# Kernel tuning notes

Measured on AMD Instinct MI355X. Metric: run time of the kernel, lower is better.

The kernel has to match this reference:

```python
import jax, jax.numpy as jnp
import numpy as np

MIN_TAU = 0.1
MAX_TAU = 10.0
DT = 0.1
HID = 64
IND = 3
B, N = 4, 262144


def _xavier(key, shape):
    fan_in, fan_out = shape[1], shape[0]
    limit = float(np.sqrt(6.0 / (fan_in + fan_out)))
    return jax.random.uniform(key, shape, jnp.float32, -limit, limit)


def setup_inputs() -> dict:
    key = jax.random.key(0)
    ks = jax.random.split(key, 7)
    h = jax.random.normal(ks[0], (B, N, HID), jnp.float32)
    u = jax.random.normal(ks[1], (B, N, IND), jnp.float32)
    return {
        "h": h,
        "u": u,
        "W_h": _xavier(ks[2], (HID, HID)),
        "U_h": _xavier(ks[3], (HID, IND)),
        "b_h": jnp.zeros((HID,), jnp.float32),
        "W_tau": _xavier(ks[4], (HID, HID)),
        "U_tau": _xavier(ks[5], (HID, IND)),
        "b_tau": jnp.zeros((HID,), jnp.float32),
        "W_out": _xavier(ks[6], (3, HID)),
        "b_out": jnp.zeros((3,), jnp.float32),
    }


def reference(h, u, W_h, U_h, b_h, W_tau, U_tau, b_tau, W_out, b_out):
    # tau: state-dependent time constant (B,N,HID)
    tau_raw = jnp.einsum('bnh,kh->bnk', h, W_tau) + jnp.einsum('bni,ki->bnk', u, U_tau) + b_tau
    tau = MIN_TAU + jax.nn.softplus(tau_raw) * (MAX_TAU - MIN_TAU)
    pre = jnp.einsum('bnh,kh->bnk', h, W_h) + jnp.einsum('bni,ki->bnk', u, U_h) + b_h
    f_h = jax.nn.sigmoid(pre)
    h_new = h + DT * (-h / tau + f_h)
    v = jnp.tanh(jnp.einsum('bnh,oh->bno', h_new, W_out) + b_out)
    return (h_new, v)
```

## Files before the change

### kernel.cpp

```cpp
#include <hip/hip_runtime.h>
#include <hip/hip_bf16.h>
#include <math.h>

#define HID 64
#define DT 0.1f
#define MIN_TAU 0.1f
#define TAU_SCALE 9.9f

#define WSTRIDE 104
#define WROWS   192
#define WELEMS  (WROWS * WSTRIDE)

typedef __attribute__((ext_vector_type(8))) short bf16x8;
typedef __attribute__((ext_vector_type(4))) float f32x4;

__device__ __forceinline__ short f2bf(float f) {
    union { __hip_bfloat16 b; short s; } c;
    c.b = __float2bfloat16(f);
    return c.s;
}
__device__ __forceinline__ float fast_rcp(float x) { return __builtin_amdgcn_rcpf(x); }
__device__ __forceinline__ float fast_tanh(float x) {
    float e = __expf(2.f * x);
    return fmaf(-2.f, fast_rcp(e + 1.f), 1.f);
}

__global__ __launch_bounds__(256) void prep_weights(
    const float* __restrict__ W_tau, const float* __restrict__ U_tau,
    const float* __restrict__ b_tau,
    const float* __restrict__ W_h, const float* __restrict__ U_h,
    const float* __restrict__ b_h,
    short* __restrict__ wbf)
{
    const int idx = blockIdx.x * 256 + threadIdx.x;
    if (idx >= WELEMS) return;
    const int row = idx / WSTRIDE;
    const int c = idx - row * WSTRIDE;
    float val = 0.f;
    if (row < 64) {
        const int r = row;
        if (c < 64)       val = W_tau[r * 64 + c];
        else if (c < 67)  val = U_tau[r * 3 + (c - 64)];
        else if (c == 67) val = b_tau[r];
    } else if (row < 128) {
        const int r = row - 64;
        if (c < 64)       val = W_h[r * 64 + c];
        else if (c < 67)  val = U_h[r * 3 + (c - 64)];
        else if (c == 67) val = b_h[r];
    } else {
        val = (c == row - 128) ? 1.0f : 0.f;
    }
    wbf[idx] = f2bf(val);
}

__global__ __launch_bounds__(256, 2) void liquid_mfma_kernel(
    const float* __restrict__ h, const float* __restrict__ u,
    const short* __restrict__ wbf,
    const float* __restrict__ W_out, const float* __restrict__ b_out,
    float* __restrict__ h_out, float* __restrict__ v_out, int ntiles)
{
    __shared__ short wlds[WELEMS];

    const int tid = threadIdx.x;
    {
        const uint4* s = (const uint4*)wbf;
        uint4* d = (uint4*)wlds;
        for (int i = tid; i < WELEMS / 8; i += 256) d[i] = s[i];
    }

    const int lane = tid & 63;
    const int col  = lane & 15;
    const int quad = lane >> 4;
    const int wid  = tid >> 6;

    float wo[3][4];
#pragma unroll
    for (int o = 0; o < 3; ++o)
#pragma unroll
        for (int nt = 0; nt < 4; ++nt)
            wo[o][nt] = W_out[o * 64 + nt * 16 + col];
    const float bo_sel = (col == 0) ? b_out[0] : ((col == 1) ? b_out[1] : b_out[2]);

    __syncthreads();

    const int tstep = gridDim.x;
    int t = blockIdx.x;

    float4 pf0, pf1, pf2, pf3;
    float pu0 = 0.f, pu1 = 0.f, pu2 = 0.f;

#define LOADA(TT)                                                              \
    do {                                                                       \
        const unsigned q_ = (unsigned)(TT) * 64u + (unsigned)(wid * 16 + col); \
        const float* hp_ = h + q_ * 64u + (unsigned)(quad * 8);                \
        pf0 = *(const float4*)hp_;                                             \
        pf1 = *(const float4*)(hp_ + 4);                                       \
        pf2 = *(const float4*)(hp_ + 32);                                      \
        pf3 = *(const float4*)(hp_ + 36);                                      \
        if (quad == 0) {                                                       \
            const float* up_ = u + q_ * 3u;                                    \
            pu0 = up_[0]; pu1 = up_[1]; pu2 = up_[2];                          \
        }                                                                      \
    } while (0)

    if (t < ntiles) LOADA(t);

    for (; t < ntiles; t += tstep) {
        const unsigned q0 = (unsigned)t * 64u + (unsigned)(wid * 16);

        bf16x8 af0, af1;
        af0[0] = f2bf(pf0.x); af0[1] = f2bf(pf0.y); af0[2] = f2bf(pf0.z); af0[3] = f2bf(pf0.w);
        af0[4] = f2bf(pf1.x); af0[5] = f2bf(pf1.y); af0[6] = f2bf(pf1.z); af0[7] = f2bf(pf1.w);
        af1[0] = f2bf(pf2.x); af1[1] = f2bf(pf2.y); af1[2] = f2bf(pf2.z); af1[3] = f2bf(pf2.w);
        af1[4] = f2bf(pf3.x); af1[5] = f2bf(pf3.y); af1[6] = f2bf(pf3.z); af1[7] = f2bf(pf3.w);

        bf16x8 af2 = (bf16x8)(short)0;
        if (quad == 0) {
            af2[0] = f2bf(pu0); af2[1] = f2bf(pu1); af2[2] = f2bf(pu2);
            af2[3] = f2bf(1.0f);
        }

        const int tn = t + tstep;
        if (tn < ntiles) LOADA(tn);

        f32x4 acc[12];
#pragma unroll
        for (int nt = 0; nt < 12; ++nt) acc[nt] = (f32x4){0.f, 0.f, 0.f, 0.f};

#pragma unroll
        for (int nt = 0; nt < 8; ++nt) {
            const short* wb = &wlds[(nt * 16 + col) * WSTRIDE + quad * 8];
            acc[nt] = __builtin_amdgcn_mfma_f32_16x16x32_bf16(
                af0, *(const bf16x8*)wb, acc[nt], 0, 0, 0);
            acc[nt] = __builtin_amdgcn_mfma_f32_16x16x32_bf16(
                af1, *(const bf16x8*)(wb + 32), acc[nt], 0, 0, 0);
            acc[nt] = __builtin_amdgcn_mfma_f32_16x16x32_bf16(
                af2, *(const bf16x8*)(wb + 64), acc[nt], 0, 0, 0);
        }
#pragma unroll
        for (int nt = 8; nt < 12; ++nt) {
            const short* wb = &wlds[(nt * 16 + col) * WSTRIDE + quad * 8];
            acc[nt] = __builtin_amdgcn_mfma_f32_16x16x32_bf16(
                af0, *(const bf16x8*)wb, acc[nt], 0, 0, 0);
            acc[nt] = __builtin_amdgcn_mfma_f32_16x16x32_bf16(
                af1, *(const bf16x8*)(wb + 32), acc[nt], 0, 0, 0);
        }

#pragma unroll
        for (int r = 0; r < 4; ++r) {
            const unsigned p = q0 + (unsigned)(quad * 4 + r);
            float pv0 = 0.f, pv1 = 0.f, pv2 = 0.f;
#pragma unroll
            for (int ntk = 0; ntk < 4; ++ntk) {
                const float at = acc[ntk][r];
                const float ap = acc[ntk + 4][r];
                const float hk = acc[ntk + 8][r];
                const float sp = fmaxf(at, 0.f) + __logf(1.f + __expf(-fabsf(at)));
                const float tau = fmaf(sp, TAU_SCALE, MIN_TAU);
                const float f = fast_rcp(1.f + __expf(-ap));
                const float hnew = fmaf(DT, f - hk * fast_rcp(tau), hk);
                h_out[p * 64u + (unsigned)(ntk * 16 + col)] = hnew;
                pv0 = fmaf(hnew, wo[0][ntk], pv0);
                pv1 = fmaf(hnew, wo[1][ntk], pv1);
                pv2 = fmaf(hnew, wo[2][ntk], pv2);
            }
#pragma unroll
            for (int s = 1; s < 16; s <<= 1) {
                pv0 += __shfl_xor(pv0, s, 64);
                pv1 += __shfl_xor(pv1, s, 64);
                pv2 += __shfl_xor(pv2, s, 64);
            }
            const float pv = (col == 0) ? pv0 : ((col == 1) ? pv1 : pv2);
            if (col < 3)
                v_out[p * 3u + (unsigned)col] = fast_tanh(pv + bo_sel);
        }
    }
#undef LOADA
}

extern "C" void kernel_launch(void* const* d_in, const int* in_sizes, int n_in,
                              void* d_out, int out_size, void* d_ws, size_t ws_size,
                              hipStream_t stream) {
    const float* h     = (const float*)d_in[0];
    const float* u     = (const float*)d_in[1];
    const float* W_h   = (const float*)d_in[2];
    const float* U_h   = (const float*)d_in[3];
    const float* b_h   = (const float*)d_in[4];
    const float* W_tau = (const float*)d_in[5];
    const float* U_tau = (const float*)d_in[6];
    const float* b_tau = (const float*)d_in[7];
    const float* W_out = (const float*)d_in[8];
    const float* b_out = (const float*)d_in[9];

    const int total = in_sizes[0] / HID;
    float* h_out = (float*)d_out;
    float* v_out = h_out + (size_t)total * HID;

    short* wbf = (short*)d_ws;

    prep_weights<<<(WELEMS + 255) / 256, 256, 0, stream>>>(
        W_tau, U_tau, b_tau, W_h, U_h, b_h, wbf);

    const int ntiles = total / 64;
    const int grid = 1024;
    liquid_mfma_kernel<<<grid, 256, 0, stream>>>(
        h, u, wbf, W_out, b_out, h_out, v_out, ntiles);
}
```

Measured before the change: 147.6 us.

## Hold weight fragments in registers and build identity transpose operands in-register

Weight B-fragments move out of LDS and are loaded once per thread into registers (24 bf16x8 vectors), which removes the LDS staging, the block barrier and the per-tile LDS reads. The identity-matrix MFMAs that transpose h into the accumulator layout now use operands generated in registers, and the wasted k-steps over zero identity columns are dropped (4 MFMAs instead of 8). The cost is a large increase in VGPR use (about 96 extra registers), which could reduce occupancy under launch_bounds(256,2) or cause spills.

```diff
diff --git a/kernel.cpp b/kernel.cpp
--- a/kernel.cpp
+++ b/kernel.cpp
@@ -8,7 +8,7 @@
 #define TAU_SCALE 9.9f
 
 #define WSTRIDE 104
-#define WROWS   192
+#define WROWS   128
 #define WELEMS  (WROWS * WSTRIDE)
 
 typedef __attribute__((ext_vector_type(8))) short bf16x8;
@@ -42,13 +42,11 @@
         if (c < 64)       val = W_tau[r * 64 + c];
         else if (c < 67)  val = U_tau[r * 3 + (c - 64)];
         else if (c == 67) val = b_tau[r];
-    } else if (row < 128) {
+    } else {
         const int r = row - 64;
         if (c < 64)       val = W_h[r * 64 + c];
         else if (c < 67)  val = U_h[r * 3 + (c - 64)];
         else if (c == 67) val = b_h[r];
-    } else {
-        val = (c == row - 128) ? 1.0f : 0.f;
     }
     wbf[idx] = f2bf(val);
 }
@@ -59,20 +57,26 @@
     const float* __restrict__ W_out, const float* __restrict__ b_out,
     float* __restrict__ h_out, float* __restrict__ v_out, int ntiles)
 {
-    __shared__ short wlds[WELEMS];
-
-    const int tid = threadIdx.x;
-    {
-        const uint4* s = (const uint4*)wbf;
-        uint4* d = (uint4*)wlds;
-        for (int i = tid; i < WELEMS / 8; i += 256) d[i] = s[i];
-    }
-
+    const int tid  = threadIdx.x;
     const int lane = tid & 63;
     const int col  = lane & 15;
     const int quad = lane >> 4;
     const int wid  = tid >> 6;
 
+    bf16x8 bw[8][3];
+#pragma unroll
+    for (int nt = 0; nt < 8; ++nt)
+#pragma unroll
+        for (int ks = 0; ks < 3; ++ks)
+            bw[nt][ks] = *(const bf16x8*)&wbf[(nt * 16 + col) * WSTRIDE + ks * 32 + quad * 8];
+
+    bf16x8 idA, idB;
+#pragma unroll
+    for (int e = 0; e < 8; ++e) {
+        idA[e] = (quad * 8 + e == col)      ? (short)0x3F80 : (short)0;
+        idB[e] = (quad * 8 + e == col + 16) ? (short)0x3F80 : (short)0;
+    }
+
     float wo[3][4];
 #pragma unroll
     for (int o = 0; o < 3; ++o)
@@ -80,8 +84,6 @@
         for (int nt = 0; nt < 4; ++nt)
             wo[o][nt] = W_out[o * 64 + nt * 16 + col];
     const float bo_sel = (col == 0) ? b_out[0] : ((col == 1) ? b_out[1] : b_out[2]);
-
-    __syncthreads();
 
     const int tstep = gridDim.x;
     int t = blockIdx.x;
@@ -129,22 +131,14 @@
 
 #pragma unroll
         for (int nt = 0; nt < 8; ++nt) {
-            const short* wb = &wlds[(nt * 16 + col) * WSTRIDE + quad * 8];
-            acc[nt] = __builtin_amdgcn_mfma_f32_16x16x32_bf16(
-                af0, *(const bf16x8*)wb, acc[nt], 0, 0, 0);
-            acc[nt] = __builtin_amdgcn_mfma_f32_16x16x32_bf16(
-                af1, *(const bf16x8*)(wb + 32), acc[nt], 0, 0, 0);
-            acc[nt] = __builtin_amdgcn_mfma_f32_16x16x32_bf16(
-                af2, *(const bf16x8*)(wb + 64), acc[nt], 0, 0, 0);
+            acc[nt] = __builtin_amdgcn_mfma_f32_16x16x32_bf16(af0, bw[nt][0], acc[nt], 0, 0, 0);
+            acc[nt] = __builtin_amdgcn_mfma_f32_16x16x32_bf16(af1, bw[nt][1], acc[nt], 0, 0, 0);
+            acc[nt] = __builtin_amdgcn_mfma_f32_16x16x32_bf16(af2, bw[nt][2], acc[nt], 0, 0, 0);
         }
-#pragma unroll
-        for (int nt = 8; nt < 12; ++nt) {
-            const short* wb = &wlds[(nt * 16 + col) * WSTRIDE + quad * 8];
-            acc[nt] = __builtin_amdgcn_mfma_f32_16x16x32_bf16(
-                af0, *(const bf16x8*)wb, acc[nt], 0, 0, 0);
-            acc[nt] = __builtin_amdgcn_mfma_f32_16x16x32_bf16(
-                af1, *(const bf16x8*)(wb + 32), acc[nt], 0, 0, 0);
-        }
+        acc[8]  = __builtin_amdgcn_mfma_f32_16x16x32_bf16(af0, idA, acc[8],  0, 0, 0);
+        acc[9]  = __builtin_amdgcn_mfma_f32_16x16x32_bf16(af0, idB, acc[9],  0, 0, 0);
+        acc[10] = __builtin_amdgcn_mfma_f32_16x16x32_bf16(af1, idA, acc[10], 0, 0, 0);
+        acc[11] = __builtin_amdgcn_mfma_f32_16x16x32_bf16(af1, idB, acc[11], 0, 0, 0);
 
 #pragma unroll
         for (int r = 0; r < 4; ++r) {
```

After: 140.2 us. -5.0%, faster.
